# Kernel tuning notes

Measured on AMD Instinct MI355X. Metric: run time of the kernel, lower is better.

The kernel has to match this reference:

```python
import jax, jax.numpy as jnp
import numpy as np
import math

B, T, C = 8, 1024, 1024
E, K = 8, 2
H = 4 * C


def new_gelu(x):
    # tanh-approx GELU, identical to the torch reference
    c = math.sqrt(2.0 / math.pi)
    return 0.5 * x * (1.0 + jnp.tanh(c * (x + 0.044715 * x ** 3)))


def setup_inputs() -> dict:
    key = jax.random.key(0)
    ks = jax.random.split(key, 4)
    x = jax.random.normal(ks[0], (B, T, C), dtype=jnp.float32)
    # router: nn.Linear(C, E, bias=False), weight [E, C], init std=0.02
    router_w = 0.02 * jax.random.normal(ks[1], (E, C), dtype=jnp.float32)
    # stacked expert MLP weights (bias=False): c_fc [E, C, H], c_proj [E, H, C]
    w_fc = 0.02 * jax.random.normal(ks[2], (E, C, H), dtype=jnp.float32)
    w_proj = 0.02 * jax.random.normal(ks[3], (E, H, C), dtype=jnp.float32)
    return {"x": x, "router_w": router_w, "w_fc": w_fc, "w_proj": w_proj}


def reference(x, router_w, w_fc, w_proj):
    n_expert = w_fc.shape[0]
    seq_rep = x.mean(axis=1)                                  # [B, C]
    router_logits = seq_rep @ router_w.T                      # [B, E]
    probs_full = jax.nn.softmax(router_logits.astype(jnp.float32), axis=-1)
    probs = probs_full.astype(x.dtype)
    weights, sel = jax.lax.top_k(probs, K)                    # [B, K]
    weights = weights / weights.sum(axis=-1, keepdims=True)

    # gather selected expert weights and run grouped dense MLPs
    w1 = w_fc[sel]                                            # [B, K, C, H]
    w2 = w_proj[sel]                                          # [B, K, H, C]
    h = new_gelu(jnp.einsum('btc,bkch->bkth', x, w1))         # [B, K, T, H]
    out_k = jnp.einsum('bkth,bkhc->bktc', h, w2)              # [B, K, T, C]
    final_output = jnp.einsum('bk,bktc->btc', weights, out_k)

    # load balancing loss
    Bf = jnp.asarray(x.shape[0], jnp.float32)
    expert_importance = probs_full.sum(axis=0) / Bf           # [E]
    is_assigned = jnp.zeros_like(probs_full).at[jnp.arange(x.shape[0])[:, None], sel].set(1.0)
    expert_load = is_assigned.sum(axis=0) / Bf                # [E]
    load_balancing_loss = n_expert * jnp.sum(expert_importance * expert_load)
    return final_output, load_balancing_loss
```

## Files before the change

kernel.cpp:

```cpp
#include <hip/hip_runtime.h>

#define B_ 8
#define T_ 1024
#define C_ 1024
#define E_ 8
#define H_ 4096

typedef float v4f __attribute__((ext_vector_type(4)));
typedef short v8s __attribute__((ext_vector_type(8)));

__device__ __forceinline__ unsigned short f2bf(float f) {
  union { float f; unsigned int u; } x; x.f = f;
  unsigned int r = x.u + 0x7fffu + ((x.u >> 16) & 1u);
  return (unsigned short)(r >> 16);
}

__device__ __forceinline__ void async_load16(const unsigned short* g, unsigned short* l) {
  __builtin_amdgcn_global_load_lds(
      (const __attribute__((address_space(1))) void*)g,
      (__attribute__((address_space(3))) void*)l, 16, 0, 0);
}


__global__ void k_meanpart(const float* __restrict__ x, float* __restrict__ part,
                           unsigned short* __restrict__ xb) {
  int b = blockIdx.x >> 5, tc = blockIdx.x & 31;
  int c4 = threadIdx.x * 4;
  const size_t base = (size_t)b * T_ * C_ + (size_t)tc * 32 * C_ + c4;
  const float* xp = x + base;
  v4f s = {0.f, 0.f, 0.f, 0.f};
  for (int t = 0; t < 32; ++t) {
    v4f v = *(const v4f*)(xp + (size_t)t * C_);
    s += v;
    ushort4 o;
    o.x = f2bf(v.x); o.y = f2bf(v.y); o.z = f2bf(v.z); o.w = f2bf(v.w);
    *(ushort4*)(xb + base + (size_t)t * C_) = o;
  }
  *(v4f*)(part + (size_t)(tc * B_ + b) * C_ + c4) = s;
}

__global__ void k_router(const float* __restrict__ part, const float* __restrict__ rw,
                         int* __restrict__ sel, float* __restrict__ wv,
                         float* __restrict__ loss_out) {
  __shared__ float seq[B_ * C_];
  __shared__ float red[B_ * E_][4];
  __shared__ float pr[B_][E_];
  __shared__ int ss[B_][2];
  const int tid = threadIdx.x;
  for (int idx = tid; idx < B_ * C_; idx += 256) {
    float s = 0.f;
#pragma unroll
    for (int tc = 0; tc < 32; ++tc) s += part[(size_t)tc * B_ * C_ + idx];
    seq[idx] = s * (1.0f / T_);
  }
  __syncthreads();
  {
    int pair = tid >> 2, sub = tid & 3;
    int b = pair >> 3, e = pair & 7;
    float acc = 0.f;
    const float* sp = seq + b * C_ + sub * 256;
    const float* wp = rw + e * C_ + sub * 256;
    for (int c = 0; c < 256; ++c) acc += sp[c] * wp[c];
    red[pair][sub] = acc;
  }
  __syncthreads();
  if (tid < B_ * E_)
    pr[tid >> 3][tid & 7] = red[tid][0] + red[tid][1] + red[tid][2] + red[tid][3];
  __syncthreads();
  if (tid < B_) {
    int b = tid;
    float mx = pr[b][0];
#pragma unroll
    for (int e = 1; e < E_; ++e) mx = fmaxf(mx, pr[b][e]);
    float p[E_]; float sum = 0.f;
#pragma unroll
    for (int e = 0; e < E_; ++e) { p[e] = __expf(pr[b][e] - mx); sum += p[e]; }
    float inv = 1.0f / sum;
#pragma unroll
    for (int e = 0; e < E_; ++e) { p[e] *= inv; pr[b][e] = p[e]; }
    int i0 = 0;
#pragma unroll
    for (int e = 1; e < E_; ++e) if (p[e] > p[i0]) i0 = e;
    int i1 = (i0 == 0) ? 1 : 0;
#pragma unroll
    for (int e = 0; e < E_; ++e) if (e != i0 && p[e] > p[i1]) i1 = e;
    float s2 = p[i0] + p[i1];
    sel[b * 2 + 0] = i0; sel[b * 2 + 1] = i1;
    wv[b * 2 + 0] = p[i0] / s2; wv[b * 2 + 1] = p[i1] / s2;
    ss[b][0] = i0; ss[b][1] = i1;
  }
  __syncthreads();
  if (tid == 0) {
    float loss = 0.f;
    for (int e = 0; e < E_; ++e) {
      float imp = 0.f, ld = 0.f;
      for (int b = 0; b < B_; ++b) {
        imp += pr[b][e];
        ld += ((ss[b][0] == e) || (ss[b][1] == e)) ? 1.f : 0.f;
      }
      loss += (imp / (float)B_) * (ld / (float)B_);
    }
    loss_out[0] = loss * (float)E_;
  }
}

__global__ void k_transpose(const float* __restrict__ src, unsigned short* __restrict__ dst,
                            int R, int Cc) {
  __shared__ float tile[64][65];
  const size_t sl = (size_t)blockIdx.z * R * Cc;
  int c0 = blockIdx.x * 64, r0 = blockIdx.y * 64;
  int tx = threadIdx.x & 15, ty = threadIdx.x >> 4;
#pragma unroll
  for (int p = 0; p < 4; ++p) {
    int r = p * 16 + ty;
    v4f v = *(const v4f*)(src + sl + (size_t)(r0 + r) * Cc + c0 + tx * 4);
    tile[r][tx * 4 + 0] = v.x; tile[r][tx * 4 + 1] = v.y;
    tile[r][tx * 4 + 2] = v.z; tile[r][tx * 4 + 3] = v.w;
  }
  __syncthreads();
#pragma unroll
  for (int p = 0; p < 4; ++p) {
    int c = p * 16 + ty;
    int rr = tx * 4;
    ushort4 o;
    o.x = f2bf(tile[rr + 0][c]); o.y = f2bf(tile[rr + 1][c]);
    o.z = f2bf(tile[rr + 2][c]); o.w = f2bf(tile[rr + 3][c]);
    *(ushort4*)(dst + sl + (size_t)(c0 + c) * R + r0 + rr) = o;
  }
}


#define BARv() __builtin_amdgcn_s_barrier()
#define LGK0() asm volatile("s_waitcnt lgkmcnt(0)" ::: "memory")
#define VMC4() asm volatile("s_waitcnt vmcnt(4)" ::: "memory")
#define VMC0() asm volatile("s_waitcnt vmcnt(0)" ::: "memory")

__device__ __forceinline__ void gemm256(const unsigned short* __restrict__ Ag,
                                        const unsigned short* __restrict__ Bg,
                                        int lda, int ldb, int Kd,
                                        unsigned short* LDS, v4f (&acc)[8][4]) {
  const int tid = threadIdx.x;
  const int lane = tid & 63;
  const int w = __builtin_amdgcn_readfirstlane(tid >> 6);
  const int wm = w >> 2, wn = w & 3;
  const int rr = lane & 15, q = lane >> 4, s7 = rr & 7;
  const int ck0 = (q ^ s7) * 8;
  const int ck1 = ((4 | q) ^ s7) * 8;
  const int aoff = wm * 8192 + rr * 64;
  const int boff = 16384 + (wn >> 1) * 8192 + (wn & 1) * 4096 + rr * 64;
  const int w8 = w * 8;
  const int l3 = lane >> 3;
  const int srow = w8 + l3;
  const int sel8 = ((lane & 7) ^ l3) * 8;
  v8s af[4][2], bfr[4][2];

#define STG(gb, ld, reg) do { \
    const unsigned short* _g = (gb) + (size_t)srow * (ld) + sel8; \
    async_load16(_g, LDS + (reg) + w8 * 64); \
    async_load16(_g + (size_t)64 * (ld), LDS + (reg) + 4096 + w8 * 64); \
  } while (0)

#define RDA(i2, qi, bs) do { \
    af[i2][0] = *(const v8s*)&LDS[(bs) + aoff + ((qi)*4+(i2))*1024 + ck0]; \
    af[i2][1] = *(const v8s*)&LDS[(bs) + aoff + ((qi)*4+(i2))*1024 + ck1]; \
  } while (0)

#define RDB(j, bs) do { \
    bfr[j][0] = *(const v8s*)&LDS[(bs) + boff + (j)*1024 + ck0]; \
    bfr[j][1] = *(const v8s*)&LDS[(bs) + boff + (j)*1024 + ck1]; \
  } while (0)

#define QUAD(qi, qj) do { \
    __builtin_amdgcn_s_setprio(1); \
    _Pragma("unroll") for (int _i = 0; _i < 4; ++_i) \
    _Pragma("unroll") for (int _j = 0; _j < 2; ++_j) { \
      acc[(qi)*4+_i][(qj)*2+_j] = __builtin_amdgcn_mfma_f32_16x16x32_bf16( \
          af[_i][0], bfr[(qj)*2+_j][0], acc[(qi)*4+_i][(qj)*2+_j], 0, 0, 0); \
      acc[(qi)*4+_i][(qj)*2+_j] = __builtin_amdgcn_mfma_f32_16x16x32_bf16( \
          af[_i][1], bfr[(qj)*2+_j][1], acc[(qi)*4+_i][(qj)*2+_j], 0, 0, 0); \
    } \
    __builtin_amdgcn_s_setprio(0); \
  } while (0)

  STG(Ag, lda, 0);
  STG(Ag + (size_t)128 * lda, lda, 8192);
  STG(Bg, ldb, 16384);
  STG(Bg + (size_t)128 * ldb, ldb, 24576);
  STG(Bg + 64, ldb, 32768 + 16384);
  STG(Bg + (size_t)128 * ldb + 64, ldb, 32768 + 24576);
  VMC4();
  BARv();

  const int NI = Kd >> 7;
  for (int I = 0; I < NI; ++I) {
    const int k0 = I << 7;
    const bool last = (I == NI - 1);
    RDA(0,0,0); RDA(1,0,0); RDA(2,0,0); RDA(3,0,0); RDB(0,0); RDB(1,0);
    STG(Ag + k0 + 64, lda, 32768 + 0);
    BARv(); LGK0(); QUAD(0,0); BARv();
    RDB(2,0); RDB(3,0);
    STG(Ag + (size_t)128 * lda + k0 + 64, lda, 32768 + 8192);
    BARv(); LGK0(); QUAD(0,1); BARv();
    RDA(0,1,0); RDA(1,1,0); RDA(2,1,0); RDA(3,1,0);
    if (!last) STG(Bg + k0 + 128, ldb, 16384);
    BARv(); LGK0(); QUAD(1,0); BARv();
    if (!last) STG(Bg + (size_t)128 * ldb + k0 + 128, ldb, 24576);
    BARv(); LGK0(); QUAD(1,1);
    if (last) { VMC0(); } else { VMC4(); }
    BARv();
    RDA(0,0,32768); RDA(1,0,32768); RDA(2,0,32768); RDA(3,0,32768);
    RDB(0,32768); RDB(1,32768);
    if (!last) STG(Ag + k0 + 128, lda, 0);
    BARv(); LGK0(); QUAD(0,0); BARv();
    RDB(2,32768); RDB(3,32768);
    if (!last) STG(Ag + (size_t)128 * lda + k0 + 128, lda, 8192);
    BARv(); LGK0(); QUAD(0,1); BARv();
    RDA(0,1,32768); RDA(1,1,32768); RDA(2,1,32768); RDA(3,1,32768);
    if (!last) STG(Bg + k0 + 192, ldb, 32768 + 16384);
    BARv(); LGK0(); QUAD(1,0); BARv();
    if (!last) STG(Bg + (size_t)128 * ldb + k0 + 192, ldb, 32768 + 24576);
    BARv(); LGK0(); QUAD(1,1);
    if (!last) VMC4();
    BARv();
  }
#undef STG
#undef RDA
#undef RDB
#undef QUAD
}

__global__ __launch_bounds__(512, 2) void k_gemm1(
    const unsigned short* __restrict__ Xb, const unsigned short* __restrict__ Wfct,
    const int* __restrict__ sel, const float* __restrict__ wv,
    unsigned short* __restrict__ Hout) {
  __shared__ unsigned short LDS[65536];
  int flat = blockIdx.x + 16 * (blockIdx.y + 4 * blockIdx.z);
  int swz = (flat & 7) * 128 + (flat >> 3);
  const int bx = swz & 15, by = (swz >> 4) & 3, bk = swz >> 6;
  const int e = sel[bk];
  const float wgt = wv[bk];
  const int row0 = by * 256, col0 = bx * 256;
  v4f acc[8][4];
#pragma unroll
  for (int i = 0; i < 8; ++i)
#pragma unroll
    for (int j = 0; j < 4; ++j) acc[i][j] = (v4f){0.f, 0.f, 0.f, 0.f};

  gemm256(Xb + (size_t)(bk >> 1) * T_ * C_ + (size_t)row0 * C_,
          Wfct + (size_t)e * H_ * C_ + (size_t)col0 * C_,
          C_, C_, C_, LDS, acc);

  const int tid = threadIdx.x;
  const int lane = tid & 63;
  const int w = tid >> 6, wm = w >> 2, wn = w & 3;
  const int rr = lane & 15, q = lane >> 4;
  unsigned short* Co = Hout + (size_t)bk * T_ * H_;
#pragma unroll
  for (int h = 0; h < 2; ++h) {
    if (wm == h) {
#pragma unroll
      for (int i = 0; i < 8; ++i)
#pragma unroll
        for (int j = 0; j < 4; ++j)
#pragma unroll
          for (int p = 0; p < 4; ++p) {
            int lr = i * 16 + q * 4 + p;
            int lc = wn * 64 + j * 16 + rr;
            float u = acc[i][j][p];
            float y = 0.7978845608028654f * (u + 0.044715f * u * u * u);
            float t = 1.0f - 2.0f / (__expf(2.0f * y) + 1.0f);
            LDS[lr * 272 + lc] = f2bf(0.5f * u * (1.0f + t) * wgt);
          }
    }
    __syncthreads();
#pragma unroll
    for (int m = 0; m < 8; ++m) {
      int idx = m * 512 + tid;
      int row = idx >> 5, cc = idx & 31;
      *(v8s*)&Co[(size_t)(row0 + h * 128 + row) * H_ + col0 + cc * 8] =
          *(const v8s*)&LDS[row * 272 + cc * 8];
    }
    __syncthreads();
  }
}

__global__ __launch_bounds__(512, 2) void k_gemm2(
    const unsigned short* __restrict__ Hin, const unsigned short* __restrict__ Wpt,
    const int* __restrict__ sel, float* __restrict__ P0, float* __restrict__ P1) {
  __shared__ unsigned short LDS[65536];
  int flat = blockIdx.x + 4 * (blockIdx.y + 4 * blockIdx.z);
  int swz = (flat & 7) * 32 + (flat >> 3);
  const int bx = swz & 3, by = (swz >> 2) & 3, bk = swz >> 4;
  const int b = bk >> 1, k = bk & 1;
  const int e = sel[bk];
  const int row0 = by * 256, col0 = bx * 256;
  v4f acc[8][4];
#pragma unroll
  for (int i = 0; i < 8; ++i)
#pragma unroll
    for (int j = 0; j < 4; ++j) acc[i][j] = (v4f){0.f, 0.f, 0.f, 0.f};

  gemm256(Hin + (size_t)bk * T_ * H_ + (size_t)row0 * H_,
          Wpt + (size_t)e * C_ * H_ + (size_t)col0 * H_,
          H_, H_, H_, LDS, acc);

  const int tid = threadIdx.x;
  const int lane = tid & 63;
  const int w = tid >> 6, wm = w >> 2, wn = w & 3;
  const int rr = lane & 15, q = lane >> 4;
  float* Co = (k == 0 ? P0 : P1) + (size_t)b * T_ * C_;
#pragma unroll
  for (int i = 0; i < 8; ++i) {
    int gr = row0 + wm * 128 + i * 16 + q * 4;
#pragma unroll
    for (int j = 0; j < 4; ++j) {
      int gc = col0 + wn * 64 + j * 16 + rr;
#pragma unroll
      for (int p = 0; p < 4; ++p)
        Co[(size_t)(gr + p) * C_ + gc] = acc[i][j][p];
    }
  }
}

__global__ void k_add(float* __restrict__ out, const float* __restrict__ p1) {
  size_t i = ((size_t)blockIdx.x * 256 + threadIdx.x) * 4;
  v4f a = *(const v4f*)(out + i);
  v4f b = *(const v4f*)(p1 + i);
  a += b;
  *(v4f*)(out + i) = a;
}


extern "C" void kernel_launch(void* const* d_in, const int* in_sizes, int n_in,
                              void* d_out, int out_size, void* d_ws, size_t ws_size,
                              hipStream_t stream) {
  const float* x   = (const float*)d_in[0];
  const float* rw  = (const float*)d_in[1];
  const float* wfc = (const float*)d_in[2];
  const float* wpj = (const float*)d_in[3];
  float* out = (float*)d_out;
  char* ws = (char*)d_ws;

  float*          part = (float*)(ws + 0);
  int*            sel  = (int*)(ws + 1048576);
  float*          wv   = (float*)(ws + 1048576 + 64);
  unsigned short* xb   = (unsigned short*)(ws + 2097152);
  unsigned short* wfct = (unsigned short*)(ws + 2097152 + 16777216);
  unsigned short* wpjt = (unsigned short*)(ws + 2097152 + 16777216 + 67108864);
  unsigned short* h    = (unsigned short*)(ws + 2097152 + 16777216 + 2*67108864ll);
  float*          p1   = (float*)(ws + 2097152);

  k_meanpart<<<dim3(B_ * 32), dim3(256), 0, stream>>>(x, part, xb);
  k_router<<<dim3(1), dim3(256), 0, stream>>>(part, rw, sel, wv,
                                              out + (size_t)B_ * T_ * C_);
  k_transpose<<<dim3(H_ / 64, C_ / 64, E_), dim3(256), 0, stream>>>(wfc, wfct, C_, H_);
  k_transpose<<<dim3(C_ / 64, H_ / 64, E_), dim3(256), 0, stream>>>(wpj, wpjt, H_, C_);

  k_gemm1<<<dim3(H_ / 256, T_ / 256, B_ * 2), dim3(512), 0, stream>>>(xb, wfct, sel, wv, h);
  k_gemm2<<<dim3(C_ / 256, T_ / 256, B_ * 2), dim3(512), 0, stream>>>(h, wpjt, sel, out, p1);
  k_add<<<dim3(B_ * T_ * C_ / 4 / 256), dim3(256), 0, stream>>>(out, p1);
}
```

Measured before the change: 653.4 us.

## Software-pipeline LDS fragment reads with double-buffered register fragments in GEMM mainloop

Restructures the 256x256 GEMM mainloop so A and B fragments are read from LDS into alternating register sets (afA/afB, bP0-bP3) one quadrant ahead of the MFMAs that use them. It drops the explicit lgkmcnt(0) waits and adds sched_barrier fences, so the LDS-read latency is meant to overlap MFMA execution. The loop is peeled into a steady-state body plus a final iteration, and global-load waits are relaxed to vmcnt(2). The epilogue LDS row stride also changes from 272 to 264 to alter bank mapping. The extra fragment registers raise VGPR pressure under launch_bounds(512,2), and correctness now depends on compiler-inserted LDS waits.

```diff
diff --git a/kernel.cpp b/kernel.cpp
--- a/kernel.cpp
+++ b/kernel.cpp
@@ -130,9 +130,10 @@
 }
 
 
-#define BARv() __builtin_amdgcn_s_barrier()
-#define LGK0() asm volatile("s_waitcnt lgkmcnt(0)" ::: "memory")
+#define BAR()  __builtin_amdgcn_s_barrier()
+#define SCH0() __builtin_amdgcn_sched_barrier(0)
 #define VMC4() asm volatile("s_waitcnt vmcnt(4)" ::: "memory")
+#define VMC2() asm volatile("s_waitcnt vmcnt(2)" ::: "memory")
 #define VMC0() asm volatile("s_waitcnt vmcnt(0)" ::: "memory")
 
 __device__ __forceinline__ void gemm256(const unsigned short* __restrict__ Ag,
@@ -152,7 +153,8 @@
   const int l3 = lane >> 3;
   const int srow = w8 + l3;
   const int sel8 = ((lane & 7) ^ l3) * 8;
-  v8s af[4][2], bfr[4][2];
+  v8s afA[4][2], afB[4][2];
+  v8s bP0[2][2], bP1[2][2], bP2[2][2], bP3[2][2];
 
 #define STG(gb, ld, reg) do { \
     const unsigned short* _g = (gb) + (size_t)srow * (ld) + sel8; \
@@ -160,26 +162,69 @@
     async_load16(_g + (size_t)64 * (ld), LDS + (reg) + 4096 + w8 * 64); \
   } while (0)
 
-#define RDA(i2, qi, bs) do { \
-    af[i2][0] = *(const v8s*)&LDS[(bs) + aoff + ((qi)*4+(i2))*1024 + ck0]; \
-    af[i2][1] = *(const v8s*)&LDS[(bs) + aoff + ((qi)*4+(i2))*1024 + ck1]; \
+#define RDA(dst, qi, bs) do { \
+    _Pragma("unroll") for (int _i = 0; _i < 4; ++_i) { \
+      dst[_i][0] = *(const v8s*)&LDS[(bs) + aoff + ((qi)*4+_i)*1024 + ck0]; \
+      dst[_i][1] = *(const v8s*)&LDS[(bs) + aoff + ((qi)*4+_i)*1024 + ck1]; \
+    } } while (0)
+
+#define RDBP(dst, qj, bs) do { \
+    _Pragma("unroll") for (int _j = 0; _j < 2; ++_j) { \
+      dst[_j][0] = *(const v8s*)&LDS[(bs) + boff + ((qj)*2+_j)*1024 + ck0]; \
+      dst[_j][1] = *(const v8s*)&LDS[(bs) + boff + ((qj)*2+_j)*1024 + ck1]; \
+    } } while (0)
+
+#define QUAD(qi, AF, BP, qj) do { \
+    __builtin_amdgcn_s_setprio(1); \
+    _Pragma("unroll") for (int _k = 0; _k < 2; ++_k) \
+    _Pragma("unroll") for (int _i = 0; _i < 4; ++_i) \
+    _Pragma("unroll") for (int _j = 0; _j < 2; ++_j) \
+      acc[(qi)*4+_i][(qj)*2+_j] = __builtin_amdgcn_mfma_f32_16x16x32_bf16( \
+          AF[_i][_k], BP[_j][_k], acc[(qi)*4+_i][(qj)*2+_j], 0, 0, 0); \
+    __builtin_amdgcn_s_setprio(0); \
   } while (0)
 
-#define RDB(j, bs) do { \
-    bfr[j][0] = *(const v8s*)&LDS[(bs) + boff + (j)*1024 + ck0]; \
-    bfr[j][1] = *(const v8s*)&LDS[(bs) + boff + (j)*1024 + ck1]; \
-  } while (0)
-
-#define QUAD(qi, qj) do { \
-    __builtin_amdgcn_s_setprio(1); \
-    _Pragma("unroll") for (int _i = 0; _i < 4; ++_i) \
-    _Pragma("unroll") for (int _j = 0; _j < 2; ++_j) { \
-      acc[(qi)*4+_i][(qj)*2+_j] = __builtin_amdgcn_mfma_f32_16x16x32_bf16( \
-          af[_i][0], bfr[(qj)*2+_j][0], acc[(qi)*4+_i][(qj)*2+_j], 0, 0, 0); \
-      acc[(qi)*4+_i][(qj)*2+_j] = __builtin_amdgcn_mfma_f32_16x16x32_bf16( \
-          af[_i][1], bfr[(qj)*2+_j][1], acc[(qi)*4+_i][(qj)*2+_j], 0, 0, 0); \
+#define ITER(k0, LAST) do { \
+     \
+    RDA(afB, 1, 0); \
+    STG(Ag + (k0) + 64, lda, 32768 + 0); \
+    STG(Ag + (size_t)128 * lda + (k0) + 64, lda, 32768 + 8192); \
+    SCH0(); BAR(); QUAD(0, afA, bP0, 0); BAR(); \
+     \
+    BAR(); QUAD(1, afB, bP0, 0); VMC4(); BAR(); SCH0(); \
+     \
+    RDBP(bP2, 0, 32768); \
+    if (!(LAST)) STG(Bg + (k0) + 128, ldb, 16384); \
+    SCH0(); BAR(); QUAD(0, afA, bP1, 1); \
+    if (LAST) { VMC0(); } else { VMC2(); } \
+    BAR(); SCH0(); \
+     \
+    RDBP(bP3, 1, 32768); \
+    RDA(afA, 0, 32768); \
+    if (!(LAST)) STG(Bg + (size_t)128 * ldb + (k0) + 128, ldb, 24576); \
+    SCH0(); BAR(); QUAD(1, afB, bP1, 1); BAR(); \
+     \
+    RDA(afB, 1, 32768); \
+    if (!(LAST)) { \
+      STG(Ag + (k0) + 128, lda, 0); \
+      STG(Ag + (size_t)128 * lda + (k0) + 128, lda, 8192); \
     } \
-    __builtin_amdgcn_s_setprio(0); \
+    SCH0(); BAR(); QUAD(0, afA, bP2, 0); BAR(); \
+     \
+    BAR(); QUAD(1, afB, bP2, 0); \
+    if (!(LAST)) VMC4(); \
+    BAR(); SCH0(); \
+     \
+    if (!(LAST)) { RDBP(bP0, 0, 0); STG(Bg + (k0) + 192, ldb, 32768 + 16384); } \
+    SCH0(); BAR(); QUAD(0, afA, bP3, 1); \
+    if (!(LAST)) VMC2(); \
+    BAR(); SCH0(); \
+     \
+    if (!(LAST)) { \
+      RDBP(bP1, 1, 0); RDA(afA, 0, 0); \
+      STG(Bg + (size_t)128 * ldb + (k0) + 192, ldb, 32768 + 24576); \
+    } \
+    SCH0(); BAR(); QUAD(1, afB, bP3, 1); BAR(); \
   } while (0)
 
   STG(Ag, lda, 0);
@@ -189,44 +234,21 @@
   STG(Bg + 64, ldb, 32768 + 16384);
   STG(Bg + (size_t)128 * ldb + 64, ldb, 32768 + 24576);
   VMC4();
-  BARv();
+  BAR(); SCH0();
+  RDA(afA, 0, 0);
+  RDBP(bP0, 0, 0);
+  RDBP(bP1, 1, 0);
 
   const int NI = Kd >> 7;
-  for (int I = 0; I < NI; ++I) {
-    const int k0 = I << 7;
-    const bool last = (I == NI - 1);
-    RDA(0,0,0); RDA(1,0,0); RDA(2,0,0); RDA(3,0,0); RDB(0,0); RDB(1,0);
-    STG(Ag + k0 + 64, lda, 32768 + 0);
-    BARv(); LGK0(); QUAD(0,0); BARv();
-    RDB(2,0); RDB(3,0);
-    STG(Ag + (size_t)128 * lda + k0 + 64, lda, 32768 + 8192);
-    BARv(); LGK0(); QUAD(0,1); BARv();
-    RDA(0,1,0); RDA(1,1,0); RDA(2,1,0); RDA(3,1,0);
-    if (!last) STG(Bg + k0 + 128, ldb, 16384);
-    BARv(); LGK0(); QUAD(1,0); BARv();
-    if (!last) STG(Bg + (size_t)128 * ldb + k0 + 128, ldb, 24576);
-    BARv(); LGK0(); QUAD(1,1);
-    if (last) { VMC0(); } else { VMC4(); }
-    BARv();
-    RDA(0,0,32768); RDA(1,0,32768); RDA(2,0,32768); RDA(3,0,32768);
-    RDB(0,32768); RDB(1,32768);
-    if (!last) STG(Ag + k0 + 128, lda, 0);
-    BARv(); LGK0(); QUAD(0,0); BARv();
-    RDB(2,32768); RDB(3,32768);
-    if (!last) STG(Ag + (size_t)128 * lda + k0 + 128, lda, 8192);
-    BARv(); LGK0(); QUAD(0,1); BARv();
-    RDA(0,1,32768); RDA(1,1,32768); RDA(2,1,32768); RDA(3,1,32768);
-    if (!last) STG(Bg + k0 + 192, ldb, 32768 + 16384);
-    BARv(); LGK0(); QUAD(1,0); BARv();
-    if (!last) STG(Bg + (size_t)128 * ldb + k0 + 192, ldb, 32768 + 24576);
-    BARv(); LGK0(); QUAD(1,1);
-    if (!last) VMC4();
-    BARv();
-  }
+#pragma unroll 1
+  for (int I = 0; I < NI - 1; ++I) ITER(I << 7, 0);
+  ITER((NI - 1) << 7, 1);
+
 #undef STG
 #undef RDA
-#undef RDB
+#undef RDBP
 #undef QUAD
+#undef ITER
 }
 
 __global__ __launch_bounds__(512, 2) void k_gemm1(
@@ -269,7 +291,7 @@
             float u = acc[i][j][p];
             float y = 0.7978845608028654f * (u + 0.044715f * u * u * u);
             float t = 1.0f - 2.0f / (__expf(2.0f * y) + 1.0f);
-            LDS[lr * 272 + lc] = f2bf(0.5f * u * (1.0f + t) * wgt);
+            LDS[lr * 264 + lc] = f2bf(0.5f * u * (1.0f + t) * wgt);
           }
     }
     __syncthreads();
@@ -278,7 +300,7 @@
       int idx = m * 512 + tid;
       int row = idx >> 5, cc = idx & 31;
       *(v8s*)&Co[(size_t)(row0 + h * 128 + row) * H_ + col0 + cc * 8] =
-          *(const v8s*)&LDS[row * 272 + cc * 8];
+          *(const v8s*)&LDS[row * 264 + cc * 8];
     }
     __syncthreads();
   }
```

Result: slower. 973.7 us (+49.0%).
